# Optimization experiments

Hardware: AMD Instinct MI355X
Metric: run time of the kernel (lower is better)

Reference implementation:

```python
import jax, jax.numpy as jnp
import numpy as np

B, S, D = 16, 577, 768
H = 12
DH = D // H  # 64


def setup_inputs() -> dict:
    key = jax.random.key(0)
    ks = jax.random.split(key, 7)
    s = 0.02
    return {
        "hidden_states": jax.random.normal(ks[0], (B, S, D), dtype=jnp.float32),
        "wq": jax.random.normal(ks[1], (D, D), dtype=jnp.float32) * s,
        "bq": jnp.zeros((D,), dtype=jnp.float32),
        "wk": jax.random.normal(ks[2], (D, D), dtype=jnp.float32) * s,
        "bk": jnp.zeros((D,), dtype=jnp.float32),
        "wv": jax.random.normal(ks[3], (D, D), dtype=jnp.float32) * s,
        "bv": jnp.zeros((D,), dtype=jnp.float32),
    }


def reference(hidden_states, wq, bq, wk, bk, wv, bv):
    # Linear projections (torch nn.Linear: x @ W^T + b)
    q = hidden_states @ wq.T + bq  # [B,S,D]
    k = hidden_states @ wk.T + bk
    v = hidden_states @ wv.T + bv

    def split_heads(x):
        return x.reshape(B, S, H, DH).transpose(0, 2, 1, 3)  # [B,H,S,DH]

    q, k, v = split_heads(q), split_heads(k), split_heads(v)
    scale = 1.0 / jnp.sqrt(jnp.float32(DH))
    scores = jnp.einsum("bhqd,bhkd->bhqk", q, k) * scale  # [B,H,S,S]
    probs = jax.nn.softmax(scores, axis=-1)
    ctx = jnp.einsum("bhqk,bhkd->bhqd", probs, v)  # [B,H,S,DH]
    ctx = ctx.transpose(0, 2, 1, 3).reshape(B, S, D)
    return ctx, probs
```

## Files before the change

kernel.cpp:

```cpp
#include <hip/hip_runtime.h>
#include <hip/hip_bf16.h>
#include <cstdint>

#define B_  16
#define S_  577
#define D_  768
#define H_  12
#define SP  640
#define M_  (B_*S_)
#define MP  9344
#define N_  2304
#define SCS 664
#define QSCALE 0.18033688011112042f

typedef __attribute__((ext_vector_type(8))) short short8;
typedef __attribute__((ext_vector_type(4))) float f32x4;

static __device__ __forceinline__ unsigned short f2bf(float f) {
    uint32_t u = __builtin_bit_cast(uint32_t, f);
    uint32_t r = u + 0x7fffu + ((u >> 16) & 1u);
    return (unsigned short)(r >> 16);
}
static __device__ __forceinline__ float bf2f(unsigned short u) {
    uint32_t x = ((uint32_t)u) << 16;
    return __builtin_bit_cast(float, x);
}

typedef unsigned int u32;
typedef __attribute__((address_space(3))) u32 lds_u32;
typedef __attribute__((address_space(1))) const u32 gbl_u32;
static __device__ __forceinline__ void gll16(const void* g, void* l) {
    __builtin_amdgcn_global_load_lds((gbl_u32*)g, (lds_u32*)l, 16, 0, 0);
}


__global__ __launch_bounds__(256) void prep(
    const float* __restrict__ X,
    const float* __restrict__ Wq, const float* __restrict__ Wk, const float* __restrict__ Wv,
    unsigned short* __restrict__ Xb, unsigned short* __restrict__ Wb,
    unsigned short* __restrict__ Vf)
{
    const int NT1 = MP * 192;
    const int NT2 = N_ * 192;
    const int VPAD = 192 * 64 * 63;
    const int total = NT1 + NT2 + VPAD;
    const int stride = gridDim.x * 256;
    for (int i = blockIdx.x * 256 + threadIdx.x; i < total; i += stride) {
        if (i < NT1) {
            int row = i / 192, c4 = i - row * 192;
            uint2 out = make_uint2(0u, 0u);
            if (row < M_) {
                float4 v = *(const float4*)(X + (size_t)row * 768 + c4 * 4);
                unsigned short p[4] = { f2bf(v.x), f2bf(v.y), f2bf(v.z), f2bf(v.w) };
                out = *(uint2*)p;
            }
            *(uint2*)(Xb + (size_t)row * 768 + c4 * 4) = out;
        } else if (i < NT1 + NT2) {
            int j = i - NT1;
            int row = j / 192, c4 = j - row * 192;
            const float* src = (row < 768) ? (Wq + (size_t)row * 768)
                             : (row < 1536) ? (Wk + (size_t)(row - 768) * 768)
                                            : (Wv + (size_t)(row - 1536) * 768);
            float4 v = *(const float4*)(src + c4 * 4);
            unsigned short p[4] = { f2bf(v.x), f2bf(v.y), f2bf(v.z), f2bf(v.w) };
            *(uint2*)(Wb + (size_t)row * 768 + c4 * 4) = *(uint2*)p;
        } else {
            int j = i - NT1 - NT2;
            int bh = j / (64 * 63), rem = j - bh * (64 * 63);
            int d = rem / 63, key = 577 + (rem - d * 63);
            size_t off = (((size_t)bh * 20 + (key >> 5)) * 4 + (d >> 4)) * 512
                       + (d & 15) * 32 + ((key >> 3) & 3) * 8 + (key & 7);
            Vf[off] = 0;
        }
    }
}

__global__ __launch_bounds__(256) void qkv_gemm(
    const unsigned short* __restrict__ Xb, const unsigned short* __restrict__ Wb,
    const float* __restrict__ bq, const float* __restrict__ bk, const float* __restrict__ bv,
    unsigned short* __restrict__ Qf, unsigned short* __restrict__ Kf,
    unsigned short* __restrict__ Vf)
{
    __shared__ unsigned short Als[128 * 64];
    __shared__ unsigned short Bls[128 * 64];

    const int mt = blockIdx.x, nt = blockIdx.y;
    const bool qk = (nt < 12);
    const int tid = threadIdx.x, lane = tid & 63, wid = tid >> 6;
    const int wm = wid >> 1, wn = wid & 1;
    const int m0 = mt * 128, n0 = nt * 128;
    const int l15 = lane & 15, g = lane >> 4;
    const int prow = lane >> 3, pc8 = lane & 7;

    const unsigned short* Pa = qk ? Bls : Als;
    const unsigned short* Pb = qk ? Als : Bls;

    f32x4 acc[4][4] = {};

    for (int kk = 0; kk < 768; kk += 64) {
        __syncthreads();
        #pragma unroll
        for (int t = 0; t < 4; ++t) {
            int row  = wid * 32 + t * 8 + prow;
            int scol = ((pc8 ^ (row & 7)) * 8);
            gll16(Xb + (size_t)(m0 + row) * 768 + kk + scol, &Als[(wid * 32 + t * 8) * 64]);
            gll16(Wb + (size_t)(n0 + row) * 768 + kk + scol, &Bls[(wid * 32 + t * 8) * 64]);
        }
        __syncthreads();

        #pragma unroll
        for (int ks = 0; ks < 2; ++ks) {
            short8 fa[4], fb[4];
            #pragma unroll
            for (int i = 0; i < 4; ++i) {
                int row = wm * 64 + i * 16 + l15;
                fa[i] = *(const short8*)&Pa[row * 64 + (((ks * 4 + g) ^ (row & 7)) * 8)];
            }
            #pragma unroll
            for (int j = 0; j < 4; ++j) {
                int row = wn * 64 + j * 16 + l15;
                fb[j] = *(const short8*)&Pb[row * 64 + (((ks * 4 + g) ^ (row & 7)) * 8)];
            }
            #pragma unroll
            for (int i = 0; i < 4; ++i)
                #pragma unroll
                for (int j = 0; j < 4; ++j)
                    acc[i][j] = __builtin_amdgcn_mfma_f32_16x16x32_bf16(fa[i], fb[j], acc[i][j], 0, 0, 0);
        }
    }

    if (qk) {
        const float* bb = (nt < 6) ? bq : bk;
        unsigned short* Dst = (nt < 6) ? Qf : Kf;
        const float scale = (nt < 6) ? QSCALE : 1.0f;
        #pragma unroll
        for (int i = 0; i < 4; ++i) {
            int nrow0 = n0 - ((nt < 6) ? 0 : 768) + wm * 64 + i * 16 + g * 4;
            float4 b4 = *(const float4*)(bb + nrow0);
            int hh = nrow0 >> 6, d0 = nrow0 & 63;
            int dh5 = d0 >> 5;
            int dsub = ((d0 >> 3) & 3) * 8 + (d0 & 7);
            #pragma unroll
            for (int j = 0; j < 4; ++j) {
                int m = m0 + wn * 64 + j * 16 + l15;
                if (m >= M_) continue;
                int b = m / 577, s = m - b * 577;
                unsigned short p[4];
                p[0] = f2bf((acc[i][j][0] + b4.x) * scale);
                p[1] = f2bf((acc[i][j][1] + b4.y) * scale);
                p[2] = f2bf((acc[i][j][2] + b4.z) * scale);
                p[3] = f2bf((acc[i][j][3] + b4.w) * scale);
                size_t off;
                if (nt < 6)
                    off = (((size_t)(b * 40 + (s >> 4)) * 12 + hh) * 2 + dh5) * 512
                        + (s & 15) * 32 + dsub;
                else
                    off = ((((size_t)(b * 12 + hh)) * 10 + (s >> 6)) * 8 + ((s >> 4) & 3) * 2 + dh5) * 512
                        + (s & 15) * 32 + dsub;
                *(uint2*)(Dst + off) = *(uint2*)p;
            }
        }
    } else {
        #pragma unroll
        for (int j = 0; j < 4; ++j) {
            int n = n0 + wn * 64 + j * 16 + l15;
            int nn = n - 1536;
            float bias = bv[nn];
            int hh = nn >> 6, dwh = nn & 63;
            #pragma unroll
            for (int i = 0; i < 4; ++i) {
                #pragma unroll
                for (int r = 0; r < 4; ++r) {
                    int m = m0 + wm * 64 + i * 16 + g * 4 + r;
                    if (m >= M_) continue;
                    int b = m / 577, s = m - b * 577;
                    float val = acc[i][j][r] + bias;
                    size_t off = (((size_t)(b * 12 + hh) * 20 + (s >> 5)) * 4 + (dwh >> 4)) * 512
                               + (dwh & 15) * 32 + ((s >> 3) & 3) * 8 + (s & 7);
                    Vf[off] = f2bf(val);
                }
            }
        }
    }
}

__global__ __launch_bounds__(256) void attn(
    const unsigned short* __restrict__ Qf, const unsigned short* __restrict__ Kf,
    const unsigned short* __restrict__ Vf,
    float* __restrict__ ctx, float* __restrict__ probs)
{
    __shared__ unsigned short sc[16 * SCS];
    __shared__ float rowinv[16];

    const int wg  = blockIdx.x;
    const int idx = (wg & 7) * 888 + (wg >> 3);
    const int bh  = idx / 37;
    const int qt  = idx - bh * 37;
    const int h   = bh % 12, b = bh / 12;

    const int tid = threadIdx.x, lane = tid & 63, wid = tid >> 6;
    const int l15 = lane & 15, g = lane >> 4;
    const int q0 = qt * 16;
    const int lofs = l15 * 32 + g * 8;

    const unsigned short* qb = Qf + ((size_t)(b * 40 + qt) * 12 + h) * 1024 + lofs;
    short8 aq0 = *(const short8*)qb;
    short8 aq1 = *(const short8*)(qb + 512);

    const unsigned short* kb0 = Kf + (size_t)bh * 40960 + wid * 1024 + lofs;
    #pragma unroll
    for (int c = 0; c < 10; ++c) {
        const unsigned short* kb = kb0 + c * 4096;
        short8 bk0 = *(const short8*)kb;
        short8 bk1 = *(const short8*)(kb + 512);
        f32x4 s4 = {};
        s4 = __builtin_amdgcn_mfma_f32_16x16x32_bf16(aq0, bk0, s4, 0, 0, 0);
        s4 = __builtin_amdgcn_mfma_f32_16x16x32_bf16(aq1, bk1, s4, 0, 0, 0);
        int key = c * 64 + wid * 16 + l15;
        #pragma unroll
        for (int r = 0; r < 4; ++r)
            sc[(g * 4 + r) * SCS + key] = (key < S_) ? f2bf(s4[r]) : (unsigned short)0xFF80u;
    }
    __syncthreads();

    const int r = tid >> 4, c0 = tid & 15;
    unsigned short* row = &sc[r * SCS];
    float m = -1e30f;
    #pragma unroll
    for (int i = 0; i < 5; ++i) {
        short8 v = *(const short8*)&row[(c0 + 16 * i) * 8];
        #pragma unroll
        for (int jj = 0; jj < 8; ++jj) m = fmaxf(m, bf2f((unsigned short)v[jj]));
    }
    #pragma unroll
    for (int o = 8; o; o >>= 1) m = fmaxf(m, __shfl_xor(m, o));

    float ssum = 0.f;
    #pragma unroll
    for (int i = 0; i < 5; ++i) {
        short8 v = *(const short8*)&row[(c0 + 16 * i) * 8];
        short8 w;
        #pragma unroll
        for (int jj = 0; jj < 8; ++jj) {
            float e = exp2f(bf2f((unsigned short)v[jj]) - m);
            ssum += e;
            w[jj] = (short)f2bf(e);
        }
        *(short8*)&row[(c0 + 16 * i) * 8] = w;
    }
    #pragma unroll
    for (int o = 8; o; o >>= 1) ssum += __shfl_xor(ssum, o);
    float inv = 1.0f / ssum;
    if (c0 == 0) rowinv[r] = inv;
    __syncthreads();

    int q = q0 + r;
    if (q < S_) {
        float* prow = probs + ((size_t)bh * S_ + q) * S_;
        #pragma unroll
        for (int i = 0; i < 5; ++i) {
            int ch = c0 + 16 * i;
            short8 v = *(const short8*)&row[ch * 8];
            if (ch < 72) {
                f32x4 o0, o1;
                o0[0] = bf2f((unsigned short)v[0]) * inv; o0[1] = bf2f((unsigned short)v[1]) * inv;
                o0[2] = bf2f((unsigned short)v[2]) * inv; o0[3] = bf2f((unsigned short)v[3]) * inv;
                o1[0] = bf2f((unsigned short)v[4]) * inv; o1[1] = bf2f((unsigned short)v[5]) * inv;
                o1[2] = bf2f((unsigned short)v[6]) * inv; o1[3] = bf2f((unsigned short)v[7]) * inv;
                __builtin_nontemporal_store(o0, (f32x4*)&prow[ch * 8]);
                __builtin_nontemporal_store(o1, (f32x4*)&prow[ch * 8 + 4]);
            } else if (ch == 72) {
                __builtin_nontemporal_store(bf2f((unsigned short)v[0]) * inv, &prow[576]);
            }
        }
    }

    f32x4 oc = {};
    const unsigned short* vb0 = Vf + (size_t)bh * 40960 + wid * 512 + lofs;
    const unsigned short* pb  = &sc[l15 * SCS + g * 8];
    #pragma unroll
    for (int kk = 0; kk < 20; ++kk) {
        short8 ap = *(const short8*)(pb + kk * 32);
        short8 bv = *(const short8*)(vb0 + kk * 2048);
        oc = __builtin_amdgcn_mfma_f32_16x16x32_bf16(ap, bv, oc, 0, 0, 0);
    }
    #pragma unroll
    for (int rr = 0; rr < 4; ++rr) {
        int qr = g * 4 + rr;
        int qq = q0 + qr;
        if (qq < S_)
            __builtin_nontemporal_store(oc[rr] * rowinv[qr],
                &ctx[((size_t)b * S_ + qq) * D_ + h * 64 + wid * 16 + l15]);
    }
}

extern "C" void kernel_launch(void* const* d_in, const int* in_sizes, int n_in,
                              void* d_out, int out_size, void* d_ws, size_t ws_size,
                              hipStream_t stream) {
    const float* X  = (const float*)d_in[0];
    const float* Wq = (const float*)d_in[1];
    const float* bq = (const float*)d_in[2];
    const float* Wk = (const float*)d_in[3];
    const float* bk = (const float*)d_in[4];
    const float* Wv = (const float*)d_in[5];
    const float* bv = (const float*)d_in[6];

    float* ctx   = (float*)d_out;
    float* probs = ctx + (size_t)B_ * S_ * D_;

    unsigned short* Xb = (unsigned short*)probs;
    unsigned short* Wb = Xb + (size_t)MP * 768;

    unsigned short* Qf = (unsigned short*)d_ws;
    unsigned short* Kf = Qf + (size_t)7864320;
    unsigned short* Vf = Kf + (size_t)7864320;

    prep<<<dim3(1024), 256, 0, stream>>>(X, Wq, Wk, Wv, Xb, Wb, Vf);
    qkv_gemm<<<dim3(73, 18), 256, 0, stream>>>(Xb, Wb, bq, bk, bv, Qf, Kf, Vf);
    attn<<<dim3(7104), 256, 0, stream>>>(Qf, Kf, Vf, ctx, probs);
}
```

Measured before the change: 213.0 us.

## Remap GEMM blocks per XCD, vectorize V padding zeroing, use raw exp in softmax

The QKV GEMM now runs on a 1D grid whose blocks are remapped so each XCD handles a contiguous run of M tiles across all N tiles, which should improve L2 reuse of the X tiles. The prep kernel zeroes the padded V tail (chunks covering keys 576..639) with 8-byte stores instead of scattered 2-byte writes. The softmax keeps the row's score vectors in registers between the max and exp passes and calls v_exp_f32 directly, skipping the range handling in exp2f. The trade-offs are extra register use in attn and no denormal or range guard on the raw exp.

```diff
diff --git a/kernel.cpp b/kernel.cpp
--- a/kernel.cpp
+++ b/kernel.cpp
@@ -25,6 +25,11 @@
     uint32_t x = ((uint32_t)u) << 16;
     return __builtin_bit_cast(float, x);
 }
+static __device__ __forceinline__ float exp2_raw(float x) {
+    float r;
+    asm("v_exp_f32 %0, %1" : "=v"(r) : "v"(x));
+    return r;
+}
 
 typedef unsigned int u32;
 typedef __attribute__((address_space(3))) u32 lds_u32;
@@ -42,7 +47,7 @@
 {
     const int NT1 = MP * 192;
     const int NT2 = N_ * 192;
-    const int VPAD = 192 * 64 * 63;
+    const int VPAD = 192 * 1024;
     const int total = NT1 + NT2 + VPAD;
     const int stride = gridDim.x * 256;
     for (int i = blockIdx.x * 256 + threadIdx.x; i < total; i += stride) {
@@ -66,11 +71,8 @@
             *(uint2*)(Wb + (size_t)row * 768 + c4 * 4) = *(uint2*)p;
         } else {
             int j = i - NT1 - NT2;
-            int bh = j / (64 * 63), rem = j - bh * (64 * 63);
-            int d = rem / 63, key = 577 + (rem - d * 63);
-            size_t off = (((size_t)bh * 20 + (key >> 5)) * 4 + (d >> 4)) * 512
-                       + (d & 15) * 32 + ((key >> 3) & 3) * 8 + (key & 7);
-            Vf[off] = 0;
+            int bh = j >> 10, rem = j & 1023;
+            *(uint2*)(Vf + (size_t)bh * 40960 + 36864 + rem * 4) = make_uint2(0u, 0u);
         }
     }
 }
@@ -84,7 +86,17 @@
     __shared__ unsigned short Als[128 * 64];
     __shared__ unsigned short Bls[128 * 64];
 
-    const int mt = blockIdx.x, nt = blockIdx.y;
+    const int bid = blockIdx.x;
+    int mt, nt;
+    if (bid < 1296) {
+        const int xcd = bid & 7, sq = bid >> 3;
+        mt = xcd * 9 + sq / 18;
+        nt = sq % 18;
+    } else {
+        mt = 72;
+        nt = bid - 1296;
+    }
+
     const bool qk = (nt < 12);
     const int tid = threadIdx.x, lane = tid & 63, wid = tid >> 6;
     const int wm = wid >> 1, wn = wid & 1;
@@ -202,6 +214,7 @@
     const int l15 = lane & 15, g = lane >> 4;
     const int q0 = qt * 16;
     const int lofs = l15 * 32 + g * 8;
+    const int r = tid >> 4, c0 = tid & 15;
 
     const unsigned short* qb = Qf + ((size_t)(b * 40 + qt) * 12 + h) * 1024 + lofs;
     short8 aq0 = *(const short8*)qb;
@@ -218,59 +231,63 @@
         s4 = __builtin_amdgcn_mfma_f32_16x16x32_bf16(aq1, bk1, s4, 0, 0, 0);
         int key = c * 64 + wid * 16 + l15;
         #pragma unroll
-        for (int r = 0; r < 4; ++r)
-            sc[(g * 4 + r) * SCS + key] = (key < S_) ? f2bf(s4[r]) : (unsigned short)0xFF80u;
+        for (int rr = 0; rr < 4; ++rr)
+            sc[(g * 4 + rr) * SCS + key] = (key < S_) ? f2bf(s4[rr]) : (unsigned short)0xFF80u;
     }
     __syncthreads();
 
-    const int r = tid >> 4, c0 = tid & 15;
-    unsigned short* row = &sc[r * SCS];
-    float m = -1e30f;
-    #pragma unroll
-    for (int i = 0; i < 5; ++i) {
-        short8 v = *(const short8*)&row[(c0 + 16 * i) * 8];
-        #pragma unroll
-        for (int jj = 0; jj < 8; ++jj) m = fmaxf(m, bf2f((unsigned short)v[jj]));
-    }
-    #pragma unroll
-    for (int o = 8; o; o >>= 1) m = fmaxf(m, __shfl_xor(m, o));
-
-    float ssum = 0.f;
-    #pragma unroll
-    for (int i = 0; i < 5; ++i) {
-        short8 v = *(const short8*)&row[(c0 + 16 * i) * 8];
-        short8 w;
-        #pragma unroll
-        for (int jj = 0; jj < 8; ++jj) {
-            float e = exp2f(bf2f((unsigned short)v[jj]) - m);
-            ssum += e;
-            w[jj] = (short)f2bf(e);
-        }
-        *(short8*)&row[(c0 + 16 * i) * 8] = w;
-    }
-    #pragma unroll
-    for (int o = 8; o; o >>= 1) ssum += __shfl_xor(ssum, o);
-    float inv = 1.0f / ssum;
-    if (c0 == 0) rowinv[r] = inv;
+    unsigned short* rowp = &sc[r * SCS];
+    float inv;
+    {
+        short8 v[5];
+        float m = -1e30f;
+        #pragma unroll
+        for (int i = 0; i < 5; ++i) {
+            v[i] = *(const short8*)&rowp[(c0 + 16 * i) * 8];
+            #pragma unroll
+            for (int jj = 0; jj < 8; ++jj) m = fmaxf(m, bf2f((unsigned short)v[i][jj]));
+        }
+        #pragma unroll
+        for (int o = 8; o; o >>= 1) m = fmaxf(m, __shfl_xor(m, o));
+
+        float ssum = 0.f;
+        #pragma unroll
+        for (int i = 0; i < 5; ++i) {
+            short8 w;
+            #pragma unroll
+            for (int jj = 0; jj < 8; ++jj) {
+                float e = exp2_raw(bf2f((unsigned short)v[i][jj]) - m);
+                ssum += e;
+                w[jj] = (short)f2bf(e);
+            }
+            *(short8*)&rowp[(c0 + 16 * i) * 8] = w;
+        }
+        #pragma unroll
+        for (int o = 8; o; o >>= 1) ssum += __shfl_xor(ssum, o);
+        inv = 1.0f / ssum;
+        if (c0 == 0) rowinv[r] = inv;
+    }
     __syncthreads();
 
-    int q = q0 + r;
-    if (q < S_) {
-        float* prow = probs + ((size_t)bh * S_ + q) * S_;
-        #pragma unroll
-        for (int i = 0; i < 5; ++i) {
-            int ch = c0 + 16 * i;
-            short8 v = *(const short8*)&row[ch * 8];
-            if (ch < 72) {
-                f32x4 o0, o1;
-                o0[0] = bf2f((unsigned short)v[0]) * inv; o0[1] = bf2f((unsigned short)v[1]) * inv;
-                o0[2] = bf2f((unsigned short)v[2]) * inv; o0[3] = bf2f((unsigned short)v[3]) * inv;
-                o1[0] = bf2f((unsigned short)v[4]) * inv; o1[1] = bf2f((unsigned short)v[5]) * inv;
-                o1[2] = bf2f((unsigned short)v[6]) * inv; o1[3] = bf2f((unsigned short)v[7]) * inv;
-                __builtin_nontemporal_store(o0, (f32x4*)&prow[ch * 8]);
-                __builtin_nontemporal_store(o1, (f32x4*)&prow[ch * 8 + 4]);
-            } else if (ch == 72) {
-                __builtin_nontemporal_store(bf2f((unsigned short)v[0]) * inv, &prow[576]);
+    {
+        int q = q0 + r;
+        if (q < S_) {
+            float* prow = probs + ((size_t)bh * S_ + q) * S_;
+            #pragma unroll
+            for (int i = 0; i < 5; ++i) {
+                int ch = c0 + 16 * i;
+                short8 v = *(const short8*)&rowp[ch * 8];
+                if (ch < 72) {
+                    f32x4 o0, o1;
+                    o0[0] = bf2f((unsigned short)v[0]) * inv; o0[1] = bf2f((unsigned short)v[1]) * inv;
+                    o0[2] = bf2f((unsigned short)v[2]) * inv; o0[3] = bf2f((unsigned short)v[3]) * inv;
+                    o1[0] = bf2f((unsigned short)v[4]) * inv; o1[1] = bf2f((unsigned short)v[5]) * inv;
+                    o1[2] = bf2f((unsigned short)v[6]) * inv; o1[3] = bf2f((unsigned short)v[7]) * inv;
+                    __builtin_nontemporal_store(o0, (f32x4*)&prow[ch * 8]);
+                    __builtin_nontemporal_store(o1, (f32x4*)&prow[ch * 8 + 4]);
+                } else if (ch == 72) {
+                    __builtin_nontemporal_store(bf2f((unsigned short)v[0]) * inv, &prow[576]);
+                }
             }
         }
     }
@@ -316,6 +333,6 @@
     unsigned short* Vf = Kf + (size_t)7864320;
 
     prep<<<dim3(1024), 256, 0, stream>>>(X, Wq, Wk, Wv, Xb, Wb, Vf);
-    qkv_gemm<<<dim3(73, 18), 256, 0, stream>>>(Xb, Wb, bq, bk, bv, Qf, Kf, Vf);
+    qkv_gemm<<<dim3(1314), 256, 0, stream>>>(Xb, Wb, bq, bk, bv, Qf, Kf, Vf);
     attn<<<dim3(7104), 256, 0, stream>>>(Qf, Kf, Vf, ctx, probs);
 }
```

New measurement: 211.3 us. Within noise of the previous version (-0.8%).
